# Performance work log

Hardware: AMD Instinct MI355X
Metric: run time of the kernel (lower is better)

## Reference

```python
import jax, jax.numpy as jnp
import numpy as np

BATCH, FIELD0, EMB = 1024, 32, 64
LAYER_SIZES = (128, 128, 128)  # split_half=True -> hidden field sizes [32, 64, 64]


def setup_inputs() -> dict:
    key = jax.random.key(0)
    ks = jax.random.split(key, 7)
    x = jax.random.normal(ks[0], (BATCH, FIELD0, EMB), dtype=jnp.float32)
    # Conv1D(kernel_size=1) weights: (in_channels=f0*fi, filters=layer_size), plus bias.
    field_sizes = [FIELD0]
    params = {}
    for i, size in enumerate(LAYER_SIZES):
        fi = field_sizes[-1]
        fan_in = FIELD0 * fi
        scale = 1.0 / np.sqrt(fan_in)
        params[f"W{i}"] = jax.random.normal(ks[1 + 2 * i], (fan_in, size), dtype=jnp.float32) * scale
        params[f"b{i}"] = jnp.zeros((size,), dtype=jnp.float32)
        field_sizes.append(size // 2 if i != len(LAYER_SIZES) - 1 else size)
    return {"x": x, **params}


def reference(x, W0, b0, W1, b1, W2, b2):
    # CIN: outer product + 1x1 conv (a matmul over the flattened field-pair axis)
    # fused as a single bilinear contraction per layer:
    #   cur[b,k,e] = sum_{i,j} x[b,i,e] * hidden[b,j,e] * W[i,j,k] + b[k]
    Ws = [(W0, b0), (W1, b1), (W2, b2)]
    f0 = x.shape[1]
    hidden = x
    final_outputs = []
    n_layers = len(Ws)
    for idx, (W, b) in enumerate(Ws):
        fi = hidden.shape[1]
        Wr = W.reshape(f0, fi, W.shape[-1])  # channel m = i*fi + j (row-major reshape)
        cur = jnp.einsum('bie,bje,ijk->bke', x, hidden, Wr) + b[None, :, None]
        # activation=None -> linear
        if idx != n_layers - 1:
            half = cur.shape[1] // 2
            hidden, direct = cur[:, :half, :], cur[:, half:, :]
        else:
            direct = cur
        final_outputs.append(direct)
    result = jnp.concatenate(final_outputs, axis=1)  # (B, 64+64+128, E)
    return jnp.sum(result, axis=-1)  # (B, 256)
```

## Files before the change

kernel.cpp:

```cpp
#include <hip/hip_runtime.h>
#include <hip/hip_bf16.h>
#include <cstdint>


typedef _Float16 half8  __attribute__((ext_vector_type(8)));
typedef _Float16 half4_ __attribute__((ext_vector_type(4)));
typedef _Float16 half2_ __attribute__((ext_vector_type(2)));
typedef float    f32x4  __attribute__((ext_vector_type(4)));

__device__ __forceinline__ unsigned short f16bits(float v) {
    return __builtin_bit_cast(unsigned short, (_Float16)v);
}

__global__ void pack_w_all(const float* __restrict__ W0, _Float16* __restrict__ Wt0,
                           const float* __restrict__ W1, _Float16* __restrict__ Wt1,
                           const float* __restrict__ W2, _Float16* __restrict__ Wt2)
{
    __shared__ _Float16 ldsT[128 * 33];
    const int blk = blockIdx.x, t = threadIdx.x;
    const float* W;
    _Float16* Wt;
    int c;
    if (blk < 32)       { W = W0; Wt = Wt0; c = blk; }
    else if (blk < 96)  { W = W1; Wt = Wt1; c = blk - 32; }
    else                { W = W2; Wt = Wt2; c = blk - 96; }

    for (int p = t; p < 32 * 128; p += 256) {
        int kk = p >> 7, m = p & 127;
        ldsT[m * 33 + kk] = (_Float16)W[(size_t)(c * 32 + kk) * 128 + m];
    }
    __syncthreads();
    int m = t >> 1, kk0 = (t & 1) * 16;
    half8 v0, v1;
#pragma unroll
    for (int i = 0; i < 8; ++i) {
        v0[i] = ldsT[m * 33 + kk0 + i];
        v1[i] = ldsT[m * 33 + kk0 + 8 + i];
    }
    *(half8*)(Wt + (size_t)c * 4096 + t * 16)     = v0;
    *(half8*)(Wt + (size_t)c * 4096 + t * 16 + 8) = v1;
}

__global__ __launch_bounds__(256, 2)
void cin_fused(const float* __restrict__ x,
               const _Float16* __restrict__ Wt0,
               const _Float16* __restrict__ Wt1,
               const float* __restrict__ bs0,
               const float* __restrict__ bs1,
               _Float16* __restrict__ S0,
               _Float16* __restrict__ S1,
               _Float16* __restrict__ S2)
{
    __shared__ alignas(16) char smem[61440];
    _Float16* slotA = (_Float16*)smem;
    _Float16* slotB = (_Float16*)(smem + 18432);
    _Float16* sX    = (_Float16*)(smem + 36864);
    _Float16* xchg  = (_Float16*)(smem + 45056);

    const int t = threadIdx.x, lane = t & 63, w = t >> 6;
    const int ks = w & 1, bb = w >> 1;
    const int lr = lane & 15, q = lane >> 4;
    const int b0 = blockIdx.x * 2;
    const int batch = b0 + bb;

    {
        const float4* xv = (const float4*)(x + (size_t)b0 * 2048);
#pragma unroll
        for (int s = 0; s < 4; ++s) {
            int p4 = t + s * 256;
            float4 v = xv[p4];
            int bb2 = p4 >> 9, idx = (p4 & 511) * 4;
            int i = idx >> 6, e0 = idx & 63;
            _Float16 h0 = (_Float16)v.x, h1 = (_Float16)v.y;
            _Float16 h2 = (_Float16)v.z, h3 = (_Float16)v.w;
            half4_ pk = {h0, h1, h2, h3};
            *(half4_*)(sX + bb2 * 2048 + i * 64 + e0) = pk;
            _Float16* hb = slotA + bb2 * 2560;
            hb[(e0 + 0) * 40 + i] = h0;
            hb[(e0 + 1) * 40 + i] = h1;
            hb[(e0 + 2) * 40 + i] = h2;
            hb[(e0 + 3) * 40 + i] = h3;
        }
    }
    __syncthreads();

    f32x4 acc[4][4];

    auto kloop = [&](const _Float16* WtL, int cBeg, int cEnd, int ish,
                     const _Float16* hbase, int ph) {
#pragma unroll
        for (int mt = 0; mt < 4; ++mt)
#pragma unroll
            for (int nt = 0; nt < 4; ++nt)
                acc[mt][nt] = f32x4{0.0f, 0.0f, 0.0f, 0.0f};
        const _Float16* aG = WtL + lr * 32 + q * 8;
        const _Float16* hP = hbase + bb * (ph << 6) + lr * ph + q * 8;
        const _Float16* xP = sX + bb * 2048 + lr;
        half8 afA[4], afB[4], hvA[4], hvB[4];
        _Float16 xsA[4], xsB[4];
        auto pf = [&](half8* af, half8* hv, _Float16* xs, int c) {
            const int i  = c >> ish;
            const int j0 = (c - (i << ish)) << 5;
            const _Float16* ag = aG + (size_t)c * 4096;
#pragma unroll
            for (int mt = 0; mt < 4; ++mt) af[mt] = *(const half8*)(ag + mt * 512);
#pragma unroll
            for (int nt = 0; nt < 4; ++nt) {
                hv[nt] = *(const half8*)(hP + nt * (ph << 4) + j0);
                xs[nt] = xP[(i << 6) + (nt << 4)];
            }
        };
        auto cp = [&](half8* af, half8* hv, _Float16* xs) {
#pragma unroll
            for (int nt = 0; nt < 4; ++nt) {
                half2_ xv2 = {xs[nt], xs[nt]};
                half8 xv8 = __builtin_shufflevector(xv2, xv2, 0, 1, 0, 1, 0, 1, 0, 1);
                half8 bf = hv[nt] * xv8;
#pragma unroll
                for (int mt = 0; mt < 4; ++mt)
                    acc[mt][nt] = __builtin_amdgcn_mfma_f32_16x16x32_f16(
                        af[mt], bf, acc[mt][nt], 0, 0, 0);
            }
        };
        pf(afA, hvA, xsA, cBeg);
        for (int c = cBeg; c < cEnd; c += 2) {
            pf(afB, hvB, xsB, c + 1);
            cp(afA, hvA, xsA);
            if (c + 2 < cEnd) pf(afA, hvA, xsA, c + 2);
            cp(afB, hvB, xsB);
        }
    };

    auto xchg_write = [&]() {
#pragma unroll
        for (int cc = 0; cc < 8; ++cc) {
            int mt = cc >> 1, n0 = (cc & 1) * 2;
            half8 hv8;
#pragma unroll
            for (int r = 0; r < 4; ++r) {
                hv8[r]     = (_Float16)acc[mt][n0][r];
                hv8[4 + r] = (_Float16)acc[mt][n0 + 1][r];
            }
            int sl = (cc + lane) & 7;
            *(half8*)(xchg + bb * 4096 + lane * 64 + sl * 8) = hv8;
        }
    };
    auto xchg_read = [&]() {
#pragma unroll
        for (int cc = 0; cc < 8; ++cc) {
            int mt = cc >> 1, n0 = (cc & 1) * 2;
            int sl = (cc + lane) & 7;
            half8 hv8 = *(const half8*)(xchg + bb * 4096 + lane * 64 + sl * 8);
#pragma unroll
            for (int r = 0; r < 4; ++r) {
                acc[mt][n0][r]     += (float)hv8[r];
                acc[mt][n0 + 1][r] += (float)hv8[4 + r];
            }
        }
    };

    auto sgemm = [&](const _Float16* hJ, int jp, int fi, _Float16* Sdst) {
        const _Float16* axp = sX + bb * 2048 + (ks * 16 + lr) * 64 + q * 8;
        const int njt = fi >> 4;
        for (int jt = 0; jt < njt; ++jt) {
            f32x4 sa = {0.0f, 0.0f, 0.0f, 0.0f};
#pragma unroll
            for (int c2 = 0; c2 < 2; ++c2) {
                half8 a = *(const half8*)(axp + c2 * 32);
                half8 b = *(const half8*)(hJ + (jt * 16 + lr) * jp + q * 8 + c2 * 32);
                sa = __builtin_amdgcn_mfma_f32_16x16x32_f16(a, b, sa, 0, 0, 0);
            }
#pragma unroll
            for (int r = 0; r < 4; ++r)
                Sdst[(size_t)batch * (32 * fi) + (ks * 16 + q * 4 + r) * fi
                     + jt * 16 + lr] = (_Float16)sa[r];
        }
    };

    sgemm(sX + bb * 2048, 64, 32, S0);
    kloop(Wt0, ks * 16, ks * 16 + 16, 0, slotA, 40);
    if (ks == 1) xchg_write();
    __syncthreads();
    if (ks == 0) {
        xchg_read();
#pragma unroll
        for (int mt = 0; mt < 4; ++mt)
#pragma unroll
            for (int nt = 0; nt < 4; ++nt) {
                int e = nt * 16 + lr;
                int j = mt * 16 + q * 4;
                half4_ vh;
#pragma unroll
                for (int r = 0; r < 4; ++r) {
                    _Float16 hval = (_Float16)(acc[mt][nt][r] + bs0[j + r]);
                    vh[r] = hval;
                    slotA[bb * 4608 + (j + r) * 72 + e] = hval;
                }
                *(half4_*)(slotB + bb * 4608 + e * 72 + j) = vh;
            }
    }
    __syncthreads();

    sgemm(slotA + bb * 4608, 72, 64, S1);
    kloop(Wt1, ks * 32, ks * 32 + 32, 1, slotB, 72);
    if (ks == 1) xchg_write();
    __syncthreads();
    if (ks == 0) {
        xchg_read();
#pragma unroll
        for (int mt = 0; mt < 4; ++mt)
#pragma unroll
            for (int nt = 0; nt < 4; ++nt) {
                int e = nt * 16 + lr;
                int j = mt * 16 + q * 4;
#pragma unroll
                for (int r = 0; r < 4; ++r)
                    slotA[bb * 4608 + (j + r) * 72 + e]
                        = (_Float16)(acc[mt][nt][r] + bs1[j + r]);
            }
    }
    __syncthreads();

    sgemm(slotA + bb * 4608, 72, 64, S2);
}

__global__ __launch_bounds__(256, 4)
void cin_direct(const _Float16* __restrict__ S0v, const _Float16* __restrict__ S1v,
                const _Float16* __restrict__ S2v,
                const _Float16* __restrict__ Wt0, const _Float16* __restrict__ Wt1,
                const _Float16* __restrict__ Wt2,
                const float* __restrict__ bs0, const float* __restrict__ bs1,
                const float* __restrict__ bs2,
                float* __restrict__ out)
{
    const int t = threadIdx.x, lane = t & 63;
    const int lr = lane & 15, q = lane >> 4;
    const int W = blockIdx.x * 4 + (t >> 6);

    const _Float16 *S, *Wt;
    const float* bias;
    int fan, nch, dm0, ob, idx;
    if (W < 256)      { S = S0v; Wt = Wt0; bias = bs0; fan = 1024; nch = 32; dm0 = 64; ob = 0;   idx = W; }
    else if (W < 512) { S = S1v; Wt = Wt1; bias = bs1; fan = 2048; nch = 64; dm0 = 64; ob = 64;  idx = W - 256; }
    else              { S = S2v; Wt = Wt2; bias = bs2; fan = 2048; nch = 64; dm0 = 0;  ob = 128; idx = W - 512; }
    const int bt = idx & 63, kt = idx >> 6;
    const int bbase = bt * 16;

    const _Float16* aG = Wt + (dm0 + kt * 16 + lr) * 32 + q * 8;
    const _Float16* bG = S + (size_t)(bbase + lr) * fan + q * 8;

    f32x4 acc = {0.0f, 0.0f, 0.0f, 0.0f};
    half8 aA = *(const half8*)(aG);
    half8 bA = *(const half8*)(bG);
    for (int c = 0; c < nch; c += 2) {
        half8 aB = *(const half8*)(aG + (size_t)(c + 1) * 4096);
        half8 bB = *(const half8*)(bG + (c + 1) * 32);
        acc = __builtin_amdgcn_mfma_f32_16x16x32_f16(aA, bA, acc, 0, 0, 0);
        if (c + 2 < nch) {
            aA = *(const half8*)(aG + (size_t)(c + 2) * 4096);
            bA = *(const half8*)(bG + (c + 2) * 32);
        }
        acc = __builtin_amdgcn_mfma_f32_16x16x32_f16(aB, bB, acc, 0, 0, 0);
    }
#pragma unroll
    for (int r = 0; r < 4; ++r) {
        int kl = kt * 16 + q * 4 + r;
        out[(size_t)(bbase + lr) * 256 + ob + kl] = acc[r] + 64.0f * bias[dm0 + kl];
    }
}

extern "C" void kernel_launch(void* const* d_in, const int* in_sizes, int n_in,
                              void* d_out, int out_size, void* d_ws, size_t ws_size,
                              hipStream_t stream)
{
    const float* x  = (const float*)d_in[0];
    const float* W0 = (const float*)d_in[1];
    const float* b0 = (const float*)d_in[2];
    const float* W1 = (const float*)d_in[3];
    const float* b1 = (const float*)d_in[4];
    const float* W2 = (const float*)d_in[5];
    const float* b2 = (const float*)d_in[6];
    float* out = (float*)d_out;

    char* ws = (char*)d_ws;
    _Float16* Wt0 = (_Float16*)(ws + 0);
    _Float16* Wt1 = (_Float16*)(ws + 262144);
    _Float16* Wt2 = (_Float16*)(ws + 786432);
    _Float16* S0  = (_Float16*)(ws + 1310720);
    _Float16* S1  = (_Float16*)(ws + 3407872);
    _Float16* S2  = (_Float16*)(ws + 7602176);
    (void)in_sizes; (void)n_in; (void)out_size; (void)ws_size;

    hipLaunchKernelGGL(pack_w_all, dim3(160), dim3(256), 0, stream,
                       W0, Wt0, W1, Wt1, W2, Wt2);

    hipLaunchKernelGGL(cin_fused, dim3(512), dim3(256), 0, stream,
                       x, Wt0, Wt1, b0, b1, S0, S1, S2);

    hipLaunchKernelGGL(cin_direct, dim3(256), dim3(256), 0, stream,
                       S0, S1, S2, Wt0, Wt1, Wt2, b0, b1, b2, out);
}
```

Measured before the change: 120.9 us.

## Fuse direct-output GEMM into CIN kernel, keeping S intermediates in LDS

Removes the separate cin_direct kernel and the global S0/S1/S2 fp16 intermediates. Each block now keeps its per-batch S tile in shared memory and computes the direct-output projections itself, loading the packed weights from global memory. The cross-wave reduction buffer is replaced by reusing slotB for partial outputs, which lowers LDS use. The cost is that the direct MFMA only fills 2 of 16 columns (two batches per block), so tensor-core work and weight traffic per useful output rise a lot, and extra barriers are added.

```diff
diff --git a/kernel.cpp b/kernel.cpp
--- a/kernel.cpp
+++ b/kernel.cpp
@@ -7,10 +7,6 @@
 typedef _Float16 half4_ __attribute__((ext_vector_type(4)));
 typedef _Float16 half2_ __attribute__((ext_vector_type(2)));
 typedef float    f32x4  __attribute__((ext_vector_type(4)));
-
-__device__ __forceinline__ unsigned short f16bits(float v) {
-    return __builtin_bit_cast(unsigned short, (_Float16)v);
-}
 
 __global__ void pack_w_all(const float* __restrict__ W0, _Float16* __restrict__ Wt0,
                            const float* __restrict__ W1, _Float16* __restrict__ Wt1,
@@ -45,23 +41,22 @@
 void cin_fused(const float* __restrict__ x,
                const _Float16* __restrict__ Wt0,
                const _Float16* __restrict__ Wt1,
+               const _Float16* __restrict__ Wt2,
                const float* __restrict__ bs0,
                const float* __restrict__ bs1,
-               _Float16* __restrict__ S0,
-               _Float16* __restrict__ S1,
-               _Float16* __restrict__ S2)
+               const float* __restrict__ bs2,
+               float* __restrict__ out)
 {
-    __shared__ alignas(16) char smem[61440];
+    __shared__ alignas(16) char smem[53248];
     _Float16* slotA = (_Float16*)smem;
     _Float16* slotB = (_Float16*)(smem + 18432);
     _Float16* sX    = (_Float16*)(smem + 36864);
-    _Float16* xchg  = (_Float16*)(smem + 45056);
+    _Float16* sS    = (_Float16*)(smem + 45056);
 
     const int t = threadIdx.x, lane = t & 63, w = t >> 6;
     const int ks = w & 1, bb = w >> 1;
     const int lr = lane & 15, q = lane >> 4;
     const int b0 = blockIdx.x * 2;
-    const int batch = b0 + bb;
 
     {
         const float4* xv = (const float4*)(x + (size_t)b0 * 2048);
@@ -131,35 +126,7 @@
         }
     };
 
-    auto xchg_write = [&]() {
-#pragma unroll
-        for (int cc = 0; cc < 8; ++cc) {
-            int mt = cc >> 1, n0 = (cc & 1) * 2;
-            half8 hv8;
-#pragma unroll
-            for (int r = 0; r < 4; ++r) {
-                hv8[r]     = (_Float16)acc[mt][n0][r];
-                hv8[4 + r] = (_Float16)acc[mt][n0 + 1][r];
-            }
-            int sl = (cc + lane) & 7;
-            *(half8*)(xchg + bb * 4096 + lane * 64 + sl * 8) = hv8;
-        }
-    };
-    auto xchg_read = [&]() {
-#pragma unroll
-        for (int cc = 0; cc < 8; ++cc) {
-            int mt = cc >> 1, n0 = (cc & 1) * 2;
-            int sl = (cc + lane) & 7;
-            half8 hv8 = *(const half8*)(xchg + bb * 4096 + lane * 64 + sl * 8);
-#pragma unroll
-            for (int r = 0; r < 4; ++r) {
-                acc[mt][n0][r]     += (float)hv8[r];
-                acc[mt][n0 + 1][r] += (float)hv8[4 + r];
-            }
-        }
-    };
-
-    auto sgemm = [&](const _Float16* hJ, int jp, int fi, _Float16* Sdst) {
+    auto sgemm = [&](const _Float16* hJ, int jp, int fi, int fan) {
         const _Float16* axp = sX + bb * 2048 + (ks * 16 + lr) * 64 + q * 8;
         const int njt = fi >> 4;
         for (int jt = 0; jt < njt; ++jt) {
@@ -172,101 +139,106 @@
             }
 #pragma unroll
             for (int r = 0; r < 4; ++r)
-                Sdst[(size_t)batch * (32 * fi) + (ks * 16 + q * 4 + r) * fi
-                     + jt * 16 + lr] = (_Float16)sa[r];
-        }
-    };
-
-    sgemm(sX + bb * 2048, 64, 32, S0);
-    kloop(Wt0, ks * 16, ks * 16 + 16, 0, slotA, 40);
-    if (ks == 1) xchg_write();
-    __syncthreads();
-    if (ks == 0) {
-        xchg_read();
+                sS[bb * fan + (ks * 16 + q * 4 + r) * fi + jt * 16 + lr]
+                    = (_Float16)sa[r];
+        }
+    };
+
+    auto direct = [&](const _Float16* WtL, int fan, int nch, int dm0, int ob,
+                      const float* biasL, int ntile) {
+        for (int tt = w; tt < ntile; tt += 4) {
+            const _Float16* aG2 = WtL + (dm0 + tt * 16 + lr) * 32 + q * 8;
+            const _Float16* bP  = sS + (lr & 1) * fan + q * 8;
+            f32x4 da = {0.0f, 0.0f, 0.0f, 0.0f};
+            half8 aA = *(const half8*)(aG2);
+            half8 bA = *(const half8*)(bP);
+            for (int c = 0; c < nch; c += 2) {
+                half8 aB = *(const half8*)(aG2 + (size_t)(c + 1) * 4096);
+                half8 bB = *(const half8*)(bP + (c + 1) * 32);
+                da = __builtin_amdgcn_mfma_f32_16x16x32_f16(aA, bA, da, 0, 0, 0);
+                if (c + 2 < nch) {
+                    aA = *(const half8*)(aG2 + (size_t)(c + 2) * 4096);
+                    bA = *(const half8*)(bP + (c + 2) * 32);
+                }
+                da = __builtin_amdgcn_mfma_f32_16x16x32_f16(aB, bB, da, 0, 0, 0);
+            }
+            if (lr < 2) {
+                int b = b0 + lr;
+#pragma unroll
+                for (int r = 0; r < 4; ++r) {
+                    int kl = tt * 16 + q * 4 + r;
+                    out[(size_t)b * 256 + ob + kl] = da[r] + 64.0f * biasL[dm0 + kl];
+                }
+            }
+        }
+    };
+
+    auto partial_out = [&](_Float16* slot) {
 #pragma unroll
         for (int mt = 0; mt < 4; ++mt)
 #pragma unroll
             for (int nt = 0; nt < 4; ++nt) {
                 int e = nt * 16 + lr;
                 int j = mt * 16 + q * 4;
+                half4_ pv;
+#pragma unroll
+                for (int r = 0; r < 4; ++r) pv[r] = (_Float16)acc[mt][nt][r];
+                *(half4_*)(slot + bb * 4608 + e * 72 + j) = pv;
+            }
+    };
+
+    sgemm(sX + bb * 2048, 64, 32, 1024);
+    __syncthreads();
+    direct(Wt0, 1024, 32, 64, 0, bs0, 4);
+    kloop(Wt0, ks * 16, ks * 16 + 16, 0, slotA, 40);
+    if (ks == 1) partial_out(slotB);
+    __syncthreads();
+    if (ks == 0) {
+#pragma unroll
+        for (int mt = 0; mt < 4; ++mt)
+#pragma unroll
+            for (int nt = 0; nt < 4; ++nt) {
+                int e = nt * 16 + lr;
+                int j = mt * 16 + q * 4;
+                half4_ pv = *(const half4_*)(slotB + bb * 4608 + e * 72 + j);
                 half4_ vh;
 #pragma unroll
                 for (int r = 0; r < 4; ++r) {
-                    _Float16 hval = (_Float16)(acc[mt][nt][r] + bs0[j + r]);
-                    vh[r] = hval;
-                    slotA[bb * 4608 + (j + r) * 72 + e] = hval;
+                    float v = acc[mt][nt][r] + (float)pv[r] + bs0[j + r];
+                    vh[r] = (_Float16)v;
+                    slotA[bb * 4608 + (j + r) * 72 + e] = (_Float16)v;
                 }
                 *(half4_*)(slotB + bb * 4608 + e * 72 + j) = vh;
             }
     }
     __syncthreads();
 
-    sgemm(slotA + bb * 4608, 72, 64, S1);
+    sgemm(slotA + bb * 4608, 72, 64, 2048);
+    __syncthreads();
+    direct(Wt1, 2048, 64, 64, 64, bs1, 4);
     kloop(Wt1, ks * 32, ks * 32 + 32, 1, slotB, 72);
-    if (ks == 1) xchg_write();
+    __syncthreads();
+    if (ks == 1) partial_out(slotB);
     __syncthreads();
     if (ks == 0) {
-        xchg_read();
 #pragma unroll
         for (int mt = 0; mt < 4; ++mt)
 #pragma unroll
             for (int nt = 0; nt < 4; ++nt) {
                 int e = nt * 16 + lr;
                 int j = mt * 16 + q * 4;
+                half4_ pv = *(const half4_*)(slotB + bb * 4608 + e * 72 + j);
 #pragma unroll
                 for (int r = 0; r < 4; ++r)
                     slotA[bb * 4608 + (j + r) * 72 + e]
-                        = (_Float16)(acc[mt][nt][r] + bs1[j + r]);
-            }
-    }
-    __syncthreads();
-
-    sgemm(slotA + bb * 4608, 72, 64, S2);
-}
-
-__global__ __launch_bounds__(256, 4)
-void cin_direct(const _Float16* __restrict__ S0v, const _Float16* __restrict__ S1v,
-                const _Float16* __restrict__ S2v,
-                const _Float16* __restrict__ Wt0, const _Float16* __restrict__ Wt1,
-                const _Float16* __restrict__ Wt2,
-                const float* __restrict__ bs0, const float* __restrict__ bs1,
-                const float* __restrict__ bs2,
-                float* __restrict__ out)
-{
-    const int t = threadIdx.x, lane = t & 63;
-    const int lr = lane & 15, q = lane >> 4;
-    const int W = blockIdx.x * 4 + (t >> 6);
-
-    const _Float16 *S, *Wt;
-    const float* bias;
-    int fan, nch, dm0, ob, idx;
-    if (W < 256)      { S = S0v; Wt = Wt0; bias = bs0; fan = 1024; nch = 32; dm0 = 64; ob = 0;   idx = W; }
-    else if (W < 512) { S = S1v; Wt = Wt1; bias = bs1; fan = 2048; nch = 64; dm0 = 64; ob = 64;  idx = W - 256; }
-    else              { S = S2v; Wt = Wt2; bias = bs2; fan = 2048; nch = 64; dm0 = 0;  ob = 128; idx = W - 512; }
-    const int bt = idx & 63, kt = idx >> 6;
-    const int bbase = bt * 16;
-
-    const _Float16* aG = Wt + (dm0 + kt * 16 + lr) * 32 + q * 8;
-    const _Float16* bG = S + (size_t)(bbase + lr) * fan + q * 8;
-
-    f32x4 acc = {0.0f, 0.0f, 0.0f, 0.0f};
-    half8 aA = *(const half8*)(aG);
-    half8 bA = *(const half8*)(bG);
-    for (int c = 0; c < nch; c += 2) {
-        half8 aB = *(const half8*)(aG + (size_t)(c + 1) * 4096);
-        half8 bB = *(const half8*)(bG + (c + 1) * 32);
-        acc = __builtin_amdgcn_mfma_f32_16x16x32_f16(aA, bA, acc, 0, 0, 0);
-        if (c + 2 < nch) {
-            aA = *(const half8*)(aG + (size_t)(c + 2) * 4096);
-            bA = *(const half8*)(bG + (c + 2) * 32);
-        }
-        acc = __builtin_amdgcn_mfma_f32_16x16x32_f16(aB, bB, acc, 0, 0, 0);
-    }
-#pragma unroll
-    for (int r = 0; r < 4; ++r) {
-        int kl = kt * 16 + q * 4 + r;
-        out[(size_t)(bbase + lr) * 256 + ob + kl] = acc[r] + 64.0f * bias[dm0 + kl];
-    }
+                        = (_Float16)(acc[mt][nt][r] + (float)pv[r] + bs1[j + r]);
+            }
+    }
+    __syncthreads();
+
+    sgemm(slotA + bb * 4608, 72, 64, 2048);
+    __syncthreads();
+    direct(Wt2, 2048, 64, 0, 128, bs2, 8);
 }
 
 extern "C" void kernel_launch(void* const* d_in, const int* in_sizes, int n_in,
@@ -286,17 +258,11 @@
     _Float16* Wt0 = (_Float16*)(ws + 0);
     _Float16* Wt1 = (_Float16*)(ws + 262144);
     _Float16* Wt2 = (_Float16*)(ws + 786432);
-    _Float16* S0  = (_Float16*)(ws + 1310720);
-    _Float16* S1  = (_Float16*)(ws + 3407872);
-    _Float16* S2  = (_Float16*)(ws + 7602176);
     (void)in_sizes; (void)n_in; (void)out_size; (void)ws_size;
 
     hipLaunchKernelGGL(pack_w_all, dim3(160), dim3(256), 0, stream,
                        W0, Wt0, W1, Wt1, W2, Wt2);
 
     hipLaunchKernelGGL(cin_fused, dim3(512), dim3(256), 0, stream,
-                       x, Wt0, Wt1, b0, b1, S0, S1, S2);
-
-    hipLaunchKernelGGL(cin_direct, dim3(256), dim3(256), 0, stream,
-                       S0, S1, S2, Wt0, Wt1, Wt2, b0, b1, b2, out);
+                       x, Wt0, Wt1, Wt2, b0, b1, b2, out);
 }
```

New measurement: 150.0 us. 1.24x slower.
